# Kernel optimization log

Hardware: AMD Instinct MI355X
Metric: run time of the kernel (lower is better)

Reference implementation:

```python
import jax, jax.numpy as jnp
import numpy as np

B, C = 8, 256
GRID = 128          # H = W = grid_size
N = GRID * GRID     # 16384 tokens
WS = 8              # swin window size
NH = 8              # num heads
DH = C // NH        # head dim = 32
HID = int(C * 4.0)  # mlp hidden = 1024
EPS = 1e-5


def _ln(x, g, b):
    m = jnp.mean(x, axis=-1, keepdims=True)
    v = jnp.mean(jnp.square(x - m), axis=-1, keepdims=True)
    return (x - m) * jax.lax.rsqrt(v + EPS) * g + b


def setup_inputs() -> dict:
    key = jax.random.key(0)
    ks = jax.random.split(key, 6)
    s = 0.02
    return {
        "x": jax.random.normal(ks[0], (B, N, C), jnp.float32),
        "ln1_g": jnp.ones((C,), jnp.float32), "ln1_b": jnp.zeros((C,), jnp.float32),
        "in_w": jax.random.normal(ks[1], (3 * C, C), jnp.float32) * s,
        "in_b": jnp.zeros((3 * C,), jnp.float32),
        "out_w": jax.random.normal(ks[2], (C, C), jnp.float32) * s,
        "out_b": jnp.zeros((C,), jnp.float32),
        "ln2_g": jnp.ones((C,), jnp.float32), "ln2_b": jnp.zeros((C,), jnp.float32),
        "w1": jax.random.normal(ks[3], (HID, C), jnp.float32) * s,
        "b1": jnp.zeros((HID,), jnp.float32),
        "w2": jax.random.normal(ks[4], (C, HID), jnp.float32) * s,
        "b2": jnp.zeros((C,), jnp.float32),
    }


def reference(x, ln1_g, ln1_b, in_w, in_b, out_w, out_b, ln2_g, ln2_b, w1, b1, w2, b2):
    shortcut = x
    xn = _ln(x, ln1_g, ln1_b)
    # window partition: [B,N,C] -> [B,H,W,C] -> [B*nW, WS*WS, C]
    xw = (xn.reshape(B, GRID // WS, WS, GRID // WS, WS, C)
            .transpose(0, 1, 3, 2, 4, 5)
            .reshape(-1, WS * WS, C))
    # torch nn.MultiheadAttention: fused in-proj, scale 1/sqrt(head_dim)
    qkv = xw @ in_w.T + in_b                      # [nW, T, 3C]
    q, k, v = jnp.split(qkv, 3, axis=-1)
    def heads(t):
        return t.reshape(t.shape[0], t.shape[1], NH, DH).transpose(0, 2, 1, 3)
    q, k, v = heads(q), heads(k), heads(v)        # [nW, NH, T, DH]
    scores = jnp.einsum('whtd,whsd->whts', q, k) * (1.0 / np.sqrt(DH))
    att = jax.nn.softmax(scores, axis=-1)
    o = jnp.einsum('whts,whsd->whtd', att, v)     # [nW, NH, T, DH]
    o = o.transpose(0, 2, 1, 3).reshape(-1, WS * WS, C)
    o = o @ out_w.T + out_b
    # window reverse: [B*nW, WS, WS, C] -> [B, N, C]
    x_attn = (o.reshape(B, GRID // WS, GRID // WS, WS, WS, C)
                .transpose(0, 1, 3, 2, 4, 5)
                .reshape(B, N, C))
    x = shortcut + x_attn
    h = _ln(x, ln2_g, ln2_b)
    h = jax.nn.gelu(h @ w1.T + b1, approximate=False)  # torch nn.GELU = exact erf
    return x + h @ w2.T + b2
```

## Files before the change

### kernel.cpp

```cpp
#include <hip/hip_runtime.h>
#include <hip/hip_bf16.h>
#include <cstdint>

#define DEVINL __device__ __forceinline__

using bf16 = __hip_bfloat16;
typedef __bf16 bf16x8 __attribute__((ext_vector_type(8)));
typedef float f32x4 __attribute__((ext_vector_type(4)));
typedef unsigned short u16x8 __attribute__((ext_vector_type(8)));

static constexpr int MTOK = 131072;

DEVINL void async_ld16(const void* g, void* l) {
  __builtin_amdgcn_global_load_lds(
      (__attribute__((address_space(1))) void*)(g),
      (__attribute__((address_space(3))) void*)(l), 16, 0, 0);
}

DEVINL unsigned short bfbits(float v) {
  bf16 h = __float2bfloat16(v);
  return *reinterpret_cast<unsigned short*>(&h);
}

DEVINL long pkaddr(long m, int k, int KP) {
  const long tile = m >> 7;
  const int row = (int)(m & 127);
  const int panel = k >> 6;
  const int c8 = ((k & 63) >> 3) ^ (row & 7);
  return ((tile * KP + panel) * 1024 + row * 8 + c8) * 8 + (k & 7);
}

__global__ __launch_bounds__(256) void cvt_w2(
    const float* __restrict__ ow, const float* __restrict__ w1,
    const float* __restrict__ w2, bf16* __restrict__ out) {
  int i = blockIdx.x * 256 + threadIdx.x;
  float v; long base; int n, k, KP;
  if (i < 65536)        { v = ow[i]; base = 0;      n = i >> 8;  k = i & 255;  KP = 4; }
  else if (i < 327680)  { int j = i - 65536;  v = w1[j]; base = 65536;  n = j >> 8;  k = j & 255;  KP = 4; }
  else                  { int j = i - 327680; v = w2[j]; base = 327680; n = j >> 10; k = j & 1023; KP = 16; }
  out[base + pkaddr(n, k, KP)] = __float2bfloat16(v);
}

template <bool REMAP>
__global__ __launch_bounds__(256) void ln_kern(
    const float* __restrict__ x, const float* __restrict__ gw,
    const float* __restrict__ bw, bf16* __restrict__ out) {
  const int lane = threadIdx.x & 63;
  const int wv = threadIdx.x >> 6;
  const long tok = (long)blockIdx.x * 4 + wv;
  const float4 v = *(const float4*)(x + tok * 256 + lane * 4);
  float s = v.x + v.y + v.z + v.w;
#pragma unroll
  for (int off = 32; off > 0; off >>= 1) s += __shfl_xor(s, off);
  const float mean = s * (1.0f / 256.0f);
  const float dx = v.x - mean, dy = v.y - mean, dz = v.z - mean, dw = v.w - mean;
  float q = dx * dx + dy * dy + dz * dz + dw * dw;
#pragma unroll
  for (int off = 32; off > 0; off >>= 1) q += __shfl_xor(q, off);
  const float inv = rsqrtf(q * (1.0f / 256.0f) + 1e-5f);
  long m;
  if (REMAP) {
    const int b = (int)(tok >> 14);
    const int n = (int)(tok & 16383);
    const int row = n >> 7, col = n & 127;
    const int w = b * 256 + (row >> 3) * 16 + (col >> 3);
    const int t = (row & 7) * 8 + (col & 7);
    m = (long)w * 64 + t;
  } else {
    m = tok;
  }
  const float4 g = *(const float4*)(gw + lane * 4);
  const float4 bb = *(const float4*)(bw + lane * 4);
  ushort4 o;
  o.x = bfbits(dx * inv * g.x + bb.x);
  o.y = bfbits(dy * inv * g.y + bb.y);
  o.z = bfbits(dz * inv * g.z + bb.z);
  o.w = bfbits(dw * inv * g.w + bb.w);
  *(ushort4*)((unsigned short*)out + pkaddr(m, lane * 4, 4)) = o;
}

enum { EPI_QKV = 0, EPI_OUTPROJ = 1, EPI_GELU = 2, EPI_RESID = 3 };

template <int KP, int EPI, bool BF32>
__global__ __launch_bounds__(256) void gemm_db(
    const bf16* __restrict__ A, const void* __restrict__ Bw,
    const float* __restrict__ bias,
    bf16* __restrict__ oQ, bf16* __restrict__ oK, bf16* __restrict__ oV,
    const float* __restrict__ resid, float* __restrict__ of32,
    bf16* __restrict__ obf) {
  __shared__ __align__(16) unsigned short smem[32768];
  const int tid = threadIdx.x;
  const int lane = tid & 63, wv = tid >> 6;
  const int quad = lane >> 4, l16 = lane & 15;
  const int wm = wv >> 1, wn = wv & 1;
  const int gx = gridDim.x;
  const int nwg = gx * gridDim.y;
  const int orig = blockIdx.x + gx * blockIdx.y;
  const int wg = (orig & 7) * (nwg >> 3) + (orig >> 3);
  const int ntile = wg % gx;
  const long mtile = wg / gx;
  const long m0 = mtile * 128;
  const int n0 = ntile * 128;

  const bf16* Bp = (const bf16*)Bw;
  const float* Bf = (const float*)Bw;
  float4 br[4][2];

  auto stageA = [&](int i, int buf) {
    const bf16* Apan = A + (mtile * KP + i) * 8192;
#pragma unroll
    for (int p = 0; p < 4; ++p) {
      const int f = p * 256 + tid;
      async_ld16(Apan + f * 8, (char*)smem + buf * 16384 + f * 16);
    }
  };
  auto stageB = [&](int i, int buf) {
    const bf16* Bpan = Bp + ((long)ntile * KP + i) * 8192;
#pragma unroll
    for (int p = 0; p < 4; ++p) {
      const int f = p * 256 + tid;
      async_ld16(Bpan + f * 8, (char*)smem + 32768 + buf * 16384 + f * 16);
    }
  };
  auto issueB = [&](int i) {
#pragma unroll
    for (int p = 0; p < 4; ++p) {
      const int f = p * 256 + tid, row = f >> 3;
      const int chunk = (f & 7) ^ (row & 7);
      const float* src = Bf + (long)(n0 + row) * 256 + i * 64 + chunk * 8;
      br[p][0] = *(const float4*)(src);
      br[p][1] = *(const float4*)(src + 4);
    }
  };
  auto writeB = [&](int buf) {
#pragma unroll
    for (int p = 0; p < 4; ++p) {
      const int f = p * 256 + tid;
      u16x8 o;
      o[0] = bfbits(br[p][0].x); o[1] = bfbits(br[p][0].y);
      o[2] = bfbits(br[p][0].z); o[3] = bfbits(br[p][0].w);
      o[4] = bfbits(br[p][1].x); o[5] = bfbits(br[p][1].y);
      o[6] = bfbits(br[p][1].z); o[7] = bfbits(br[p][1].w);
      *(u16x8*)((char*)smem + 32768 + buf * 16384 + f * 16) = o;
    }
  };

  const f32x4 fz = {0.f, 0.f, 0.f, 0.f};
  f32x4 acc[4][4];
#pragma unroll
  for (int a = 0; a < 4; ++a) {
#pragma unroll
    for (int b = 0; b < 4; ++b) acc[a][b] = fz;
  }

  if constexpr (BF32) { issueB(0); stageA(0, 0); }
  else                { stageA(0, 0); stageB(0, 0); }

#pragma unroll 1
  for (int i = 0; i < KP; ++i) {
    if constexpr (BF32) writeB(i & 1);
    __syncthreads();
    if (i + 1 < KP) {
      if constexpr (BF32) { issueB(i + 1); stageA(i + 1, (i + 1) & 1); }
      else                { stageA(i + 1, (i + 1) & 1); stageB(i + 1, (i + 1) & 1); }
    }
    const unsigned short* Asb = smem + (i & 1) * 8192;
    const unsigned short* Bsb = smem + 16384 + (i & 1) * 8192;
#pragma unroll
    for (int kk = 0; kk < 2; ++kk) {
      bf16x8 af[4], bfr[4];
#pragma unroll
      for (int mt = 0; mt < 4; ++mt) {
        const int row = wm * 64 + mt * 16 + l16;
        const int c8 = (kk * 4 + quad) ^ (row & 7);
        af[mt] = *(const bf16x8*)(Asb + row * 64 + c8 * 8);
      }
#pragma unroll
      for (int nt = 0; nt < 4; ++nt) {
        const int row = wn * 64 + nt * 16 + l16;
        const int c8 = (kk * 4 + quad) ^ (row & 7);
        bfr[nt] = *(const bf16x8*)(Bsb + row * 64 + c8 * 8);
      }
#pragma unroll
      for (int mt = 0; mt < 4; ++mt) {
#pragma unroll
        for (int nt = 0; nt < 4; ++nt) {
          acc[mt][nt] = __builtin_amdgcn_mfma_f32_16x16x32_bf16(
              af[mt], bfr[nt], acc[mt][nt], 0, 0, 0);
        }
      }
    }
  }

  if constexpr (EPI == EPI_QKV || EPI == EPI_GELU) {
    const int region = (EPI == EPI_QKV) ? (n0 >> 8) : 0;
    float bj4[4];
#pragma unroll
    for (int nt = 0; nt < 4; ++nt) bj4[nt] = bias[n0 + wn * 64 + nt * 16 + l16];
    __syncthreads();
    if (EPI == EPI_GELU || region < 2) {
#pragma unroll
      for (int mt = 0; mt < 4; ++mt) {
#pragma unroll
        for (int nt = 0; nt < 4; ++nt) {
          const int j_l = wn * 64 + nt * 16 + l16;
#pragma unroll
          for (int r = 0; r < 4; ++r) {
            const int m_l = wm * 64 + mt * 16 + quad * 4 + r;
            float v = acc[mt][nt][r] + bj4[nt];
            if constexpr (EPI == EPI_GELU)
              v = 0.5f * v * (1.0f + erff(v * 0.70710678118654752f));
            smem[m_l * 136 + j_l] = bfbits(v);
          }
        }
      }
    } else {
#pragma unroll
      for (int mt = 0; mt < 4; ++mt) {
#pragma unroll
        for (int nt = 0; nt < 4; ++nt) {
          const int j_l = wn * 64 + nt * 16 + l16;
          const int m_b = wm * 64 + mt * 16 + quad * 4;
          ushort4 pk;
          pk.x = bfbits(acc[mt][nt][0] + bj4[nt]);
          pk.y = bfbits(acc[mt][nt][1] + bj4[nt]);
          pk.z = bfbits(acc[mt][nt][2] + bj4[nt]);
          pk.w = bfbits(acc[mt][nt][3] + bj4[nt]);
          *(ushort4*)(smem + j_l * 136 + m_b) = pk;
        }
      }
    }
    __syncthreads();
    if constexpr (EPI == EPI_QKV) {
      bf16* dst0 = (region == 0) ? oQ : ((region == 1) ? oK : oV);
      const int hbase = (n0 >> 5) & 7;
      const long w0 = m0 >> 6;
      if (region < 2) {
#pragma unroll
        for (int p = 0; p < 8; ++p) {
          const int u = p * 256 + tid;
          const int c = u >> 8, rr = u & 255;
          const int t = rr >> 2, d0 = (rr & 3) * 8;
          const unsigned short* src = smem + ((c >> 2) * 64 + t) * 136 + (c & 3) * 32 + d0;
          const long hb = (w0 + (c >> 2)) * 8 + hbase + (c & 3);
          *(u16x8*)((unsigned short*)dst0 + (hb * 64 + t) * 32 + d0) = *(const u16x8*)src;
        }
      } else {
#pragma unroll
        for (int p = 0; p < 8; ++p) {
          const int u = p * 256 + tid;
          const int c = u >> 8, rr = u & 255;
          const int d = rr >> 3, t0 = (rr & 7) * 8;
          const unsigned short* src = smem + ((c & 3) * 32 + d) * 136 + (c >> 2) * 64 + t0;
          const long hb = (w0 + (c >> 2)) * 8 + hbase + (c & 3);
          *(u16x8*)((unsigned short*)dst0 + (hb * 32 + d) * 64 + t0) = *(const u16x8*)src;
        }
      }
    } else {
      const int p0 = n0 >> 6;
#pragma unroll
      for (int p = 0; p < 8; ++p) {
        const int u = p * 256 + tid;
        const int p_l = u >> 10, g = u & 1023;
        const int row = g >> 3, c8 = g & 7;
        const unsigned short* src = smem + row * 136 + p_l * 64 + ((c8 ^ (row & 7)) * 8);
        unsigned short* dst = (unsigned short*)obf + ((mtile * 16 + p0 + p_l) * 1024 + g) * 8;
        *(u16x8*)dst = *(const u16x8*)src;
      }
    }
  } else {
#pragma unroll
    for (int mt = 0; mt < 4; ++mt) {
#pragma unroll
      for (int nt = 0; nt < 4; ++nt) {
        const long mb = m0 + wm * 64 + mt * 16 + quad * 4;
        const int j = n0 + wn * 64 + nt * 16 + l16;
        const float bj = bias[j];
#pragma unroll
        for (int r = 0; r < 4; ++r) {
          const long m = mb + r;
          const float v = acc[mt][nt][r] + bj;
          if constexpr (EPI == EPI_OUTPROJ) {
            const int w = (int)(m >> 6), t = (int)(m & 63);
            const int b = w >> 8, wi = w & 255;
            const int row = (wi >> 4) * 8 + (t >> 3);
            const int col = (wi & 15) * 8 + (t & 7);
            const long addr = ((long)b * 16384 + row * 128 + col) * 256 + j;
            of32[addr] = v + resid[addr];
          } else {
            const long addr = m * 256 + j;
            of32[addr] += v;
          }
        }
      }
    }
  }
}

__global__ __launch_bounds__(256) void attn_kern(
    const bf16* __restrict__ Qb, const bf16* __restrict__ Kb,
    const bf16* __restrict__ Vtb, bf16* __restrict__ O) {
  __shared__ __align__(16) unsigned short P[4][64 * 72];
  __shared__ __align__(16) unsigned short Cw[4][64 * 72];
  const int lane = threadIdx.x & 63;
  const int wv = threadIdx.x >> 6;
  const int quad = lane >> 4, l16 = lane & 15;
  const long w = blockIdx.x;
  unsigned short* Pw = &P[wv][0];
  unsigned short* Cww = &Cw[wv][0];
  const float SC = 0.17677669529663689f;
  const f32x4 fz = {0.f, 0.f, 0.f, 0.f};

#pragma unroll 1
  for (int hi = 0; hi < 2; ++hi) {
    const int h = wv * 2 + hi;
    const bf16* qp = Qb + ((w * 8 + h) * 64) * 32;
    const bf16* kp = Kb + ((w * 8 + h) * 64) * 32;
    const bf16* vt = Vtb + ((w * 8 + h) * 32) * 64;

    bf16x8 qf[4], kf[4];
#pragma unroll
    for (int mt = 0; mt < 4; ++mt)
      qf[mt] = *(const bf16x8*)(qp + (mt * 16 + l16) * 32 + quad * 8);
#pragma unroll
    for (int nt = 0; nt < 4; ++nt)
      kf[nt] = *(const bf16x8*)(kp + (nt * 16 + l16) * 32 + quad * 8);

    f32x4 s[4][4];
#pragma unroll
    for (int a = 0; a < 4; ++a) {
#pragma unroll
      for (int b = 0; b < 4; ++b) s[a][b] = fz;
    }
#pragma unroll
    for (int mt = 0; mt < 4; ++mt) {
#pragma unroll
      for (int nt = 0; nt < 4; ++nt) {
        s[mt][nt] = __builtin_amdgcn_mfma_f32_16x16x32_bf16(qf[mt], kf[nt],
                                                            s[mt][nt], 0, 0, 0);
      }
    }

#pragma unroll
    for (int mt = 0; mt < 4; ++mt) {
#pragma unroll
      for (int r = 0; r < 4; ++r) {
        float a0 = s[mt][0][r] * SC, a1 = s[mt][1][r] * SC;
        float a2 = s[mt][2][r] * SC, a3 = s[mt][3][r] * SC;
        float mx = fmaxf(fmaxf(a0, a1), fmaxf(a2, a3));
#pragma unroll
        for (int off = 8; off > 0; off >>= 1) mx = fmaxf(mx, __shfl_xor(mx, off));
        a0 = __expf(a0 - mx); a1 = __expf(a1 - mx);
        a2 = __expf(a2 - mx); a3 = __expf(a3 - mx);
        float sm = a0 + a1 + a2 + a3;
#pragma unroll
        for (int off = 8; off > 0; off >>= 1) sm += __shfl_xor(sm, off);
        const float iv = 1.0f / sm;
        const int rp = (mt * 16 + quad * 4 + r) * 72;
        Pw[rp + l16]      = bfbits(a0 * iv);
        Pw[rp + 16 + l16] = bfbits(a1 * iv);
        Pw[rp + 32 + l16] = bfbits(a2 * iv);
        Pw[rp + 48 + l16] = bfbits(a3 * iv);
      }
    }

    bf16x8 vf[2][2];
#pragma unroll
    for (int kt = 0; kt < 2; ++kt) {
#pragma unroll
      for (int dt = 0; dt < 2; ++dt)
        vf[kt][dt] = *(const bf16x8*)(vt + (dt * 16 + l16) * 64 + kt * 32 + quad * 8);
    }
    f32x4 oa[4][2];
#pragma unroll
    for (int a = 0; a < 4; ++a) { oa[a][0] = fz; oa[a][1] = fz; }
#pragma unroll
    for (int mt = 0; mt < 4; ++mt) {
      const unsigned short* pr = Pw + (mt * 16 + l16) * 72 + quad * 8;
      const bf16x8 p0 = *(const bf16x8*)(pr);
      const bf16x8 p1 = *(const bf16x8*)(pr + 32);
#pragma unroll
      for (int dt = 0; dt < 2; ++dt) {
        oa[mt][dt] = __builtin_amdgcn_mfma_f32_16x16x32_bf16(p0, vf[0][dt], oa[mt][dt], 0, 0, 0);
        oa[mt][dt] = __builtin_amdgcn_mfma_f32_16x16x32_bf16(p1, vf[1][dt], oa[mt][dt], 0, 0, 0);
      }
    }

#pragma unroll
    for (int mt = 0; mt < 4; ++mt) {
#pragma unroll
      for (int dt = 0; dt < 2; ++dt) {
#pragma unroll
        for (int r = 0; r < 4; ++r) {
          const int m_l = mt * 16 + quad * 4 + r;
          const int j_l = hi * 32 + dt * 16 + l16;
          Cww[m_l * 72 + j_l] = bfbits(oa[mt][dt][r]);
        }
      }
    }
  }

  __syncthreads();
  const long tile = w >> 1;
  const int half = (int)(w & 1);
#pragma unroll
  for (int p = 0; p < 8; ++p) {
    const int u = p * 64 + lane;
    const int row = u >> 3, c8 = u & 7;
    const unsigned short* src = Cww + row * 72 + ((c8 ^ (row & 7)) * 8);
    unsigned short* dst = (unsigned short*)O +
        ((tile * 4 + wv) * 1024 + (half * 64 + row) * 8 + c8) * 8;
    *(u16x8*)dst = *(const u16x8*)src;
  }
}

extern "C" void kernel_launch(void* const* d_in, const int* in_sizes, int n_in,
                              void* d_out, int out_size, void* d_ws, size_t ws_size,
                              hipStream_t stream) {
  const float* x     = (const float*)d_in[0];
  const float* ln1g  = (const float*)d_in[1];
  const float* ln1b  = (const float*)d_in[2];
  const float* in_w  = (const float*)d_in[3];
  const float* in_b  = (const float*)d_in[4];
  const float* out_w = (const float*)d_in[5];
  const float* out_b = (const float*)d_in[6];
  const float* ln2g  = (const float*)d_in[7];
  const float* ln2b  = (const float*)d_in[8];
  const float* w1    = (const float*)d_in[9];
  const float* b1    = (const float*)d_in[10];
  const float* w2    = (const float*)d_in[11];
  const float* b2    = (const float*)d_in[12];
  float* out = (float*)d_out;

  char* ws = (char*)d_ws;
  const size_t MB = 1ull << 20;
  bf16* XW   = (bf16*)ws;
  bf16* Qb   = (bf16*)(ws + 64 * MB);
  bf16* Kb   = (bf16*)(ws + 128 * MB);
  bf16* Vtb  = (bf16*)(ws + 192 * MB);
  bf16* WB   = (bf16*)(ws + 64 * MB);
  bf16* Wo   = WB;
  bf16* W1c  = WB + 65536;
  bf16* W2c  = WB + 327680;
  bf16* H1   = (bf16*)(ws + 66 * MB);
  bf16* Obuf = XW;
  bf16* Hbuf = XW;

  ln_kern<true><<<MTOK / 4, 256, 0, stream>>>(x, ln1g, ln1b, XW);
  gemm_db<4, EPI_QKV, true><<<dim3(6, MTOK / 128), 256, 0, stream>>>(
      XW, in_w, in_b, Qb, Kb, Vtb, nullptr, nullptr, nullptr);
  attn_kern<<<2048, 256, 0, stream>>>(Qb, Kb, Vtb, Obuf);
  cvt_w2<<<2304, 256, 0, stream>>>(out_w, w1, w2, WB);
  gemm_db<4, EPI_OUTPROJ, false><<<dim3(2, MTOK / 128), 256, 0, stream>>>(
      Obuf, Wo, out_b, nullptr, nullptr, nullptr, x, out, nullptr);
  ln_kern<false><<<MTOK / 4, 256, 0, stream>>>(out, ln2g, ln2b, Hbuf);
  for (int c = 0; c < 2; ++c) {
    gemm_db<4, EPI_GELU, false><<<dim3(8, 512), 256, 0, stream>>>(
        Hbuf + (long)c * 16777216, W1c, b1,
        nullptr, nullptr, nullptr, nullptr, nullptr, H1);
    gemm_db<16, EPI_RESID, false><<<dim3(2, 512), 256, 0, stream>>>(
        H1, W2c, b2, nullptr, nullptr, nullptr, nullptr,
        out + (long)c * 16777216, nullptr);
  }
}
```

Before: 812.0 us.

## Fuse MLP fc1+GELU+fc2 into one kernel keeping hidden activations in LDS

Replaces the chunked two-GEMM MLP (fc1 with GELU epilogue writing a bf16 hidden buffer, then fc2 reading it back) with a single kernel per 128-token tile. The kernel keeps the LN2 output resident in LDS, streams W1/W2 tiles through a double buffer, and computes GELU into an LDS staging buffer consumed directly by the second GEMM, accumulating all 256 output columns in registers. This removes the round trip of the 1024-wide hidden activations through global memory and several launches. In exchange it uses 128 KB of LDS at one block per CU, with heavy register pressure from three accumulator sets, and its only overlap comes from the double-buffered weight loads.

```diff
diff --git a/kernel.cpp b/kernel.cpp
--- a/kernel.cpp
+++ b/kernel.cpp
@@ -192,13 +192,13 @@
     }
   }
 
-  if constexpr (EPI == EPI_QKV || EPI == EPI_GELU) {
-    const int region = (EPI == EPI_QKV) ? (n0 >> 8) : 0;
+  if constexpr (EPI == EPI_QKV) {
+    const int region = n0 >> 8;
     float bj4[4];
 #pragma unroll
     for (int nt = 0; nt < 4; ++nt) bj4[nt] = bias[n0 + wn * 64 + nt * 16 + l16];
     __syncthreads();
-    if (EPI == EPI_GELU || region < 2) {
+    if (region < 2) {
 #pragma unroll
       for (int mt = 0; mt < 4; ++mt) {
 #pragma unroll
@@ -207,10 +207,7 @@
 #pragma unroll
           for (int r = 0; r < 4; ++r) {
             const int m_l = wm * 64 + mt * 16 + quad * 4 + r;
-            float v = acc[mt][nt][r] + bj4[nt];
-            if constexpr (EPI == EPI_GELU)
-              v = 0.5f * v * (1.0f + erff(v * 0.70710678118654752f));
-            smem[m_l * 136 + j_l] = bfbits(v);
+            smem[m_l * 136 + j_l] = bfbits(acc[mt][nt][r] + bj4[nt]);
           }
         }
       }
@@ -231,41 +228,28 @@
       }
     }
     __syncthreads();
-    if constexpr (EPI == EPI_QKV) {
-      bf16* dst0 = (region == 0) ? oQ : ((region == 1) ? oK : oV);
-      const int hbase = (n0 >> 5) & 7;
-      const long w0 = m0 >> 6;
-      if (region < 2) {
-#pragma unroll
-        for (int p = 0; p < 8; ++p) {
-          const int u = p * 256 + tid;
-          const int c = u >> 8, rr = u & 255;
-          const int t = rr >> 2, d0 = (rr & 3) * 8;
-          const unsigned short* src = smem + ((c >> 2) * 64 + t) * 136 + (c & 3) * 32 + d0;
-          const long hb = (w0 + (c >> 2)) * 8 + hbase + (c & 3);
-          *(u16x8*)((unsigned short*)dst0 + (hb * 64 + t) * 32 + d0) = *(const u16x8*)src;
-        }
-      } else {
-#pragma unroll
-        for (int p = 0; p < 8; ++p) {
-          const int u = p * 256 + tid;
-          const int c = u >> 8, rr = u & 255;
-          const int d = rr >> 3, t0 = (rr & 7) * 8;
-          const unsigned short* src = smem + ((c & 3) * 32 + d) * 136 + (c >> 2) * 64 + t0;
-          const long hb = (w0 + (c >> 2)) * 8 + hbase + (c & 3);
-          *(u16x8*)((unsigned short*)dst0 + (hb * 32 + d) * 64 + t0) = *(const u16x8*)src;
-        }
-      }
-    } else {
-      const int p0 = n0 >> 6;
+    bf16* dst0 = (region == 0) ? oQ : ((region == 1) ? oK : oV);
+    const int hbase = (n0 >> 5) & 7;
+    const long w0 = m0 >> 6;
+    if (region < 2) {
 #pragma unroll
       for (int p = 0; p < 8; ++p) {
         const int u = p * 256 + tid;
-        const int p_l = u >> 10, g = u & 1023;
-        const int row = g >> 3, c8 = g & 7;
-        const unsigned short* src = smem + row * 136 + p_l * 64 + ((c8 ^ (row & 7)) * 8);
-        unsigned short* dst = (unsigned short*)obf + ((mtile * 16 + p0 + p_l) * 1024 + g) * 8;
-        *(u16x8*)dst = *(const u16x8*)src;
+        const int c = u >> 8, rr = u & 255;
+        const int t = rr >> 2, d0 = (rr & 3) * 8;
+        const unsigned short* src = smem + ((c >> 2) * 64 + t) * 136 + (c & 3) * 32 + d0;
+        const long hb = (w0 + (c >> 2)) * 8 + hbase + (c & 3);
+        *(u16x8*)((unsigned short*)dst0 + (hb * 64 + t) * 32 + d0) = *(const u16x8*)src;
+      }
+    } else {
+#pragma unroll
+      for (int p = 0; p < 8; ++p) {
+        const int u = p * 256 + tid;
+        const int c = u >> 8, rr = u & 255;
+        const int d = rr >> 3, t0 = (rr & 7) * 8;
+        const unsigned short* src = smem + ((c & 3) * 32 + d) * 136 + (c >> 2) * 64 + t0;
+        const long hb = (w0 + (c >> 2)) * 8 + hbase + (c & 3);
+        *(u16x8*)((unsigned short*)dst0 + (hb * 32 + d) * 64 + t0) = *(const u16x8*)src;
       }
     }
   } else {
@@ -292,6 +276,164 @@
             of32[addr] += v;
           }
         }
+      }
+    }
+  }
+}
+
+__global__ __launch_bounds__(256, 1) void mlp_fused(
+    const bf16* __restrict__ A, const bf16* __restrict__ W1p,
+    const bf16* __restrict__ W2p, const float* __restrict__ b1,
+    const float* __restrict__ b2, float* __restrict__ out) {
+  __shared__ __align__(16) unsigned short smem[65536];
+  unsigned short* Ares = smem;
+  unsigned short* Wbuf = smem + 32768;
+  unsigned short* Pbuf = smem + 49152;
+  const int tid = threadIdx.x;
+  const int lane = tid & 63;
+  const int wv = tid >> 6;
+  const int quad = lane >> 4, l16 = lane & 15;
+  const int wm = wv >> 1, wn = wv & 1;
+  const long mtile = blockIdx.x;
+
+  auto stageW = [&](const bf16* wp, int buf) {
+#pragma unroll
+    for (int c = 0; c < 4; ++c) {
+      const int f = c * 256 + tid;
+      async_ld16(wp + f * 8, (char*)(Wbuf + buf * 8192) + f * 16);
+    }
+  };
+  auto wptr = [&](int u) -> const bf16* {
+    const int hcu = u >> 3, su = u & 7;
+    return (su < 4) ? W1p + (hcu * 4 + su) * 8192
+                    : W2p + ((((su >= 6) ? 16 : 0) + hcu * 2 + (su & 1))) * 8192;
+  };
+  auto mm = [&](const unsigned short* Abase, const unsigned short* Bbase,
+                int arow0, int brow0, f32x4 (&acc)[4][4]) {
+#pragma unroll
+    for (int kk = 0; kk < 2; ++kk) {
+      bf16x8 af[4], bfr[4];
+#pragma unroll
+      for (int x = 0; x < 4; ++x) {
+        const int row = arow0 + x * 16 + l16;
+        const int c8 = (kk * 4 + quad) ^ (row & 7);
+        af[x] = *(const bf16x8*)(Abase + row * 64 + c8 * 8);
+      }
+#pragma unroll
+      for (int x = 0; x < 4; ++x) {
+        const int row = brow0 + x * 16 + l16;
+        const int c8 = (kk * 4 + quad) ^ (row & 7);
+        bfr[x] = *(const bf16x8*)(Bbase + row * 64 + c8 * 8);
+      }
+#pragma unroll
+      for (int a = 0; a < 4; ++a) {
+#pragma unroll
+        for (int b = 0; b < 4; ++b) {
+          acc[a][b] = __builtin_amdgcn_mfma_f32_16x16x32_bf16(
+              af[a], bfr[b], acc[a][b], 0, 0, 0);
+        }
+      }
+    }
+  };
+
+  {
+    const bf16* Ap = A + mtile * 32768;
+#pragma unroll
+    for (int c = 0; c < 16; ++c) {
+      const int f = c * 256 + tid;
+      async_ld16(Ap + f * 8, (char*)Ares + f * 16);
+    }
+    stageW(W1p, 0);
+  }
+
+  const f32x4 fz = {0.f, 0.f, 0.f, 0.f};
+  f32x4 acc2a[4][4], acc2b[4][4];
+#pragma unroll
+  for (int a = 0; a < 4; ++a) {
+#pragma unroll
+    for (int b = 0; b < 4; ++b) { acc2a[a][b] = fz; acc2b[a][b] = fz; }
+  }
+
+#pragma unroll 1
+  for (int hc = 0; hc < 8; ++hc) {
+    f32x4 acc1[4][4];
+#pragma unroll
+    for (int a = 0; a < 4; ++a) {
+#pragma unroll
+      for (int b = 0; b < 4; ++b) acc1[a][b] = fz;
+    }
+    f32x4 b1v[4];
+#pragma unroll
+    for (int s = 0; s < 4; ++s) {
+      const int t = hc * 8 + s;
+      __syncthreads();
+      stageW(wptr(t + 1), (t + 1) & 1);
+      if (s == 2) {
+#pragma unroll
+        for (int x = 0; x < 4; ++x)
+          b1v[x] = *(const f32x4*)(b1 + hc * 128 + wn * 64 + x * 16 + quad * 4);
+      }
+      mm(Wbuf + (t & 1) * 8192, Ares + s * 8192, wn * 64, wm * 64, acc1);
+    }
+#pragma unroll
+    for (int ht = 0; ht < 4; ++ht) {
+#pragma unroll
+      for (int mt = 0; mt < 4; ++mt) {
+        const int m_l = wm * 64 + mt * 16 + l16;
+        ushort4 pk;
+#pragma unroll
+        for (int r = 0; r < 4; ++r) {
+          const float v = acc1[ht][mt][r] + b1v[ht][r];
+          const float g = 0.5f * v * (1.0f + erff(v * 0.70710678118654752f));
+          ((unsigned short*)&pk)[r] = bfbits(g);
+        }
+        const int c8p = (ht * 2 + (quad >> 1)) ^ (m_l & 7);
+        *(ushort4*)(Pbuf + wn * 8192 + m_l * 64 + c8p * 8 + (quad & 1) * 4) = pk;
+      }
+    }
+    {
+      const int t = hc * 8 + 4;
+      __syncthreads();
+      stageW(wptr(t + 1), (t + 1) & 1);
+      mm(Pbuf, Wbuf + (t & 1) * 8192, wm * 64, wn * 64, acc2a);
+    }
+    {
+      const int t = hc * 8 + 5;
+      __syncthreads();
+      stageW(wptr(t + 1), (t + 1) & 1);
+      mm(Pbuf + 8192, Wbuf + (t & 1) * 8192, wm * 64, wn * 64, acc2a);
+    }
+    {
+      const int t = hc * 8 + 6;
+      __syncthreads();
+      stageW(wptr(t + 1), (t + 1) & 1);
+      mm(Pbuf, Wbuf + (t & 1) * 8192, wm * 64, wn * 64, acc2b);
+    }
+    {
+      const int t = hc * 8 + 7;
+      __syncthreads();
+      if (t + 1 < 64) stageW(wptr(t + 1), (t + 1) & 1);
+      mm(Pbuf + 8192, Wbuf + (t & 1) * 8192, wm * 64, wn * 64, acc2b);
+    }
+  }
+
+  const long m0 = mtile * 128;
+  float b2a[4], b2b[4];
+#pragma unroll
+  for (int nt = 0; nt < 4; ++nt) {
+    b2a[nt] = b2[wn * 64 + nt * 16 + l16];
+    b2b[nt] = b2[128 + wn * 64 + nt * 16 + l16];
+  }
+#pragma unroll
+  for (int mt = 0; mt < 4; ++mt) {
+#pragma unroll
+    for (int nt = 0; nt < 4; ++nt) {
+      const long mb = m0 + wm * 64 + mt * 16 + quad * 4;
+      const int ja = wn * 64 + nt * 16 + l16;
+#pragma unroll
+      for (int r = 0; r < 4; ++r) {
+        out[(mb + r) * 256 + ja] += acc2a[mt][nt][r] + b2a[nt];
+        out[(mb + r) * 256 + ja + 128] += acc2b[mt][nt][r] + b2b[nt];
       }
     }
   }
@@ -442,7 +584,6 @@
   bf16* Wo   = WB;
   bf16* W1c  = WB + 65536;
   bf16* W2c  = WB + 327680;
-  bf16* H1   = (bf16*)(ws + 66 * MB);
   bf16* Obuf = XW;
   bf16* Hbuf = XW;
 
@@ -454,12 +595,5 @@
   gemm_db<4, EPI_OUTPROJ, false><<<dim3(2, MTOK / 128), 256, 0, stream>>>(
       Obuf, Wo, out_b, nullptr, nullptr, nullptr, x, out, nullptr);
   ln_kern<false><<<MTOK / 4, 256, 0, stream>>>(out, ln2g, ln2b, Hbuf);
-  for (int c = 0; c < 2; ++c) {
-    gemm_db<4, EPI_GELU, false><<<dim3(8, 512), 256, 0, stream>>>(
-        Hbuf + (long)c * 16777216, W1c, b1,
-        nullptr, nullptr, nullptr, nullptr, nullptr, H1);
-    gemm_db<16, EPI_RESID, false><<<dim3(2, 512), 256, 0, stream>>>(
-        H1, W2c, b2, nullptr, nullptr, nullptr, nullptr,
-        out + (long)c * 16777216, nullptr);
-  }
-}
+  mlp_fused<<<MTOK / 128, 256, 0, stream>>>(Hbuf, W1c, W2c, b1, b2, out);
+}
```

Measured after the change: 822.1 us. Within noise of the previous version (+1.2%).
